# Kernel optimization log

Measured on AMD Instinct MI355X. Metric: run time of the kernel, lower is better.

Reference implementation:

```python
import jax, jax.numpy as jnp
import numpy as np

IN_F, OUT_F = 64, 32
N = IN_F * OUT_F + OUT_F  # 2080 sampled parameters (weights + bias)
B, S = 8, 2048
SCALE_INIT = 1.0 * float(np.sqrt(2.0 / (IN_F + OUT_F)))


def setup_inputs() -> dict:
    key = jax.random.key(0)
    k_x, k_eps, k_loc, k_cov = jax.random.split(key, 4)
    x = jax.random.normal(k_x, (B, S, IN_F), dtype=jnp.float32)
    eps = jax.random.normal(k_eps, (B, S, N), dtype=jnp.float32)
    loc = 0.01 * jax.random.normal(k_loc, (N,), dtype=jnp.float32)
    logvar = jnp.full((N,), float(np.log(SCALE_INIT)), dtype=jnp.float32)
    n_off = N * (N - 1) // 2
    cov_flat = 0.001 * jax.random.normal(k_cov, (n_off,), dtype=jnp.float32)
    return {"x": x, "eps": eps, "loc": loc, "logvar": logvar, "cov_flat": cov_flat}


def reference(x, eps, loc, logvar, cov_flat):
    n = loc.shape[0]
    in_f = x.shape[-1]
    out_f = n // (in_f + 1)  # n = out*(in+1)
    # flat_to_triangular (strictly lower) + make_cholesky, vectorized scatter
    rows, cols = np.tril_indices(n, -1)
    A = jnp.zeros((n, n), dtype=x.dtype).at[rows, cols].set(cov_flat)
    L = A + jnp.diag(jnp.exp(logvar * 0.5))  # off-diag from cov, diag = std
    # MultivariateNormal rsample: loc + L @ eps (per batch sample)
    W = loc + jnp.einsum('bsn,mn->bsm', eps, L)  # [B,S,N]
    b = W[..., :out_f]
    Wm = W[..., out_f:].reshape(*W.shape[:-1], in_f, out_f)  # [B,S,in,out]
    y = jnp.einsum('bsh,bshk->bsk', x, Wm) + b
    return y
```

## Files before the change

### kernel.cpp

```cpp
#include <hip/hip_runtime.h>
#include <hip/hip_bf16.h>

#define IN_F  64
#define OUT_F 32
#define NV    2080
#define NPAD  2176
#define MM    16384
#define KK    2080
#define NBN   17

typedef __attribute__((ext_vector_type(4))) float f32x4;
typedef __bf16 bf16x8 __attribute__((ext_vector_type(8)));

using gas_ptr = const __attribute__((address_space(1))) void*;
using lds_ptr = __attribute__((address_space(3))) void*;

__global__ __launch_bounds__(256) void build_L_k(const float* __restrict__ cov,
                                                 const float* __restrict__ logvar,
                                                 __hip_bfloat16* __restrict__ LB) {
    const int idx = blockIdx.x * 256 + threadIdx.x;
    const int m = idx / KK;
    const int k = idx - m * KK;
    float v = 0.0f;
    if (m < NV) {
        if (k < m)       v = cov[(size_t)(m * (m - 1) / 2) + k];
        else if (k == m) v = expf(0.5f * logvar[m]);
    }
    LB[idx] = __float2bfloat16(v);
}

__global__ __launch_bounds__(256) void gemm_zl_k(const float* __restrict__ A,
                                                 const __hip_bfloat16* __restrict__ BT,
                                                 const float* __restrict__ loc,
                                                 const float* __restrict__ x,
                                                 float* __restrict__ Ypart) {
    __shared__ __align__(16) __hip_bfloat16 As[2][128 * 32];
    __shared__ __align__(16) __hip_bfloat16 Bs[2][128 * 32];
    __shared__ float xs[128][4];

    const int tid  = threadIdx.x;
    const int bm   = blockIdx.x;
    const int bn   = (NBN - 1) - blockIdx.y;
    const int wave = tid >> 6;
    const int lane = tid & 63;
    const int quad = lane >> 4;
    const int r16  = lane & 15;

    const int kblocks = min(KK / 32, 4 * bn + 4);

    {
        const int tl = tid >> 1;
        const int cc = (tid & 1) * 2;
#pragma unroll
        for (int c = cc; c < cc + 2; c++) {
            const int h = 4 * bn - 1 + c;
            float w = 0.0f;
            if (bn == 0 && c == 0)          w = 1.0f;
            else if (h >= 0 && h < IN_F)    w = x[(size_t)(bm * 128 + tl) * IN_F + h];
            xs[tl][c] = w;
        }
    }

    const float*          Ag = A  + (size_t)bm * 128 * KK;
    const __hip_bfloat16* Bg = BT + (size_t)bn * 128 * KK;

    const int c0 = tid, c1 = tid + 256;
    const int ar0 = c0 >> 2, ap0 = (c0 & 3) ^ ((ar0 >> 1) & 3);
    const int ar1 = c1 >> 2, ap1 = (c1 & 3) ^ ((ar1 >> 1) & 3);
    const size_t gofs0 = (size_t)ar0 * KK + ap0 * 8;
    const size_t gofs1 = (size_t)ar1 * KK + ap1 * 8;

    f32x4 acc[2][8];
#pragma unroll
    for (int i = 0; i < 2; i++)
#pragma unroll
        for (int j = 0; j < 8; j++) acc[i][j] = f32x4{0.f, 0.f, 0.f, 0.f};

    int aofs[2], bofs[8];
#pragma unroll
    for (int i = 0; i < 2; i++) {
        const int arow = 32 * wave + 16 * i + r16;
        aofs[i] = arow * 32 + (quad ^ ((arow >> 1) & 3)) * 8;
    }
#pragma unroll
    for (int j = 0; j < 8; j++) {
        const int brow = 16 * j + r16;
        bofs[j] = brow * 32 + (quad ^ ((brow >> 1) & 3)) * 8;
    }

    {
        f32x4 ra0 = *(const f32x4*)(Ag + gofs0);
        f32x4 ra1 = *(const f32x4*)(Ag + gofs0 + 4);
        f32x4 ra2 = *(const f32x4*)(Ag + gofs1);
        f32x4 ra3 = *(const f32x4*)(Ag + gofs1 + 4);
        __builtin_amdgcn_global_load_lds((gas_ptr)(Bg + gofs0), (lds_ptr)(&Bs[0][0] + c0 * 8), 16, 0, 0);
        __builtin_amdgcn_global_load_lds((gas_ptr)(Bg + gofs1), (lds_ptr)(&Bs[0][0] + c1 * 8), 16, 0, 0);
        bf16x8 w0, w1;
#pragma unroll
        for (int q = 0; q < 4; q++) {
            w0[q] = (__bf16)ra0[q]; w0[4 + q] = (__bf16)ra1[q];
            w1[q] = (__bf16)ra2[q]; w1[4 + q] = (__bf16)ra3[q];
        }
        *(bf16x8*)(&As[0][0] + c0 * 8) = w0;
        *(bf16x8*)(&As[0][0] + c1 * 8) = w1;
    }

    for (int kb = 0; kb < kblocks; ++kb) {
        const int cur = kb & 1;
        __syncthreads();

        const bool pf = (kb + 1 < kblocks);
        f32x4 ra0, ra1, ra2, ra3;
        if (pf) {
            const size_t k0 = (size_t)(kb + 1) * 32;
            ra0 = *(const f32x4*)(Ag + k0 + gofs0);
            ra1 = *(const f32x4*)(Ag + k0 + gofs0 + 4);
            ra2 = *(const f32x4*)(Ag + k0 + gofs1);
            ra3 = *(const f32x4*)(Ag + k0 + gofs1 + 4);
            __builtin_amdgcn_global_load_lds((gas_ptr)(Bg + k0 + gofs0), (lds_ptr)(&Bs[cur ^ 1][0] + c0 * 8), 16, 0, 0);
            __builtin_amdgcn_global_load_lds((gas_ptr)(Bg + k0 + gofs1), (lds_ptr)(&Bs[cur ^ 1][0] + c1 * 8), 16, 0, 0);
        }

        bf16x8 af[2], bfr[8];
#pragma unroll
        for (int i = 0; i < 2; i++) af[i]  = *(const bf16x8*)(&As[cur][0] + aofs[i]);
#pragma unroll
        for (int j = 0; j < 8; j++) bfr[j] = *(const bf16x8*)(&Bs[cur][0] + bofs[j]);
#pragma unroll
        for (int i = 0; i < 2; i++)
#pragma unroll
            for (int j = 0; j < 8; j++)
                acc[i][j] = __builtin_amdgcn_mfma_f32_16x16x32_bf16(af[i], bfr[j], acc[i][j], 0, 0, 0);

        if (pf) {
            bf16x8 w0, w1;
#pragma unroll
            for (int q = 0; q < 4; q++) {
                w0[q] = (__bf16)ra0[q]; w0[4 + q] = (__bf16)ra1[q];
                w1[q] = (__bf16)ra2[q]; w1[4 + q] = (__bf16)ra3[q];
            }
            *(bf16x8*)(&As[cur ^ 1][0] + c0 * 8) = w0;
            *(bf16x8*)(&As[cur ^ 1][0] + c1 * 8) = w1;
        }
    }

    float locv[8];
#pragma unroll
    for (int j = 0; j < 8; j++) {
        const int col = bn * 128 + 16 * j + r16;
        locv[j] = (col < NV) ? loc[col] : 0.0f;
    }

    float* yp = Ypart + ((size_t)bn * MM + (size_t)bm * 128) * OUT_F;
#pragma unroll
    for (int i = 0; i < 2; i++) {
#pragma unroll
        for (int r = 0; r < 4; r++) {
            const int tl = 32 * wave + 16 * i + 4 * quad + r;
            float v0 = 0.0f, v1 = 0.0f;
#pragma unroll
            for (int c = 0; c < 4; c++) {
                const float w = xs[tl][c];
                v0 += w * (acc[i][2 * c][r]     + locv[2 * c]);
                v1 += w * (acc[i][2 * c + 1][r] + locv[2 * c + 1]);
            }
            yp[(size_t)tl * OUT_F + r16]      = v0;
            yp[(size_t)tl * OUT_F + 16 + r16] = v1;
        }
    }
}

__global__ __launch_bounds__(256) void reduce_y_k(const float4* __restrict__ yp,
                                                  float4* __restrict__ y) {
    const size_t i = (size_t)blockIdx.x * 256 + threadIdx.x;
    float4 s = yp[i];
#pragma unroll
    for (int b = 1; b < NBN; b++) {
        float4 v = yp[i + (size_t)b * (MM * OUT_F / 4)];
        s.x += v.x; s.y += v.y; s.z += v.z; s.w += v.w;
    }
    y[i] = s;
}

extern "C" void kernel_launch(void* const* d_in, const int* in_sizes, int n_in,
                              void* d_out, int out_size, void* d_ws, size_t ws_size,
                              hipStream_t stream) {
    const float* x      = (const float*)d_in[0];
    const float* eps    = (const float*)d_in[1];
    const float* loc    = (const float*)d_in[2];
    const float* logvar = (const float*)d_in[3];
    const float* cov    = (const float*)d_in[4];
    float* y = (float*)d_out;

    char* ws = (char*)d_ws;
    __hip_bfloat16* LB    = (__hip_bfloat16*)ws;
    float*          Ypart = (float*)(ws + (size_t)NPAD * KK * 2);

    build_L_k<<<(NPAD * KK) / 256, 256, 0, stream>>>(cov, logvar, LB);
    gemm_zl_k<<<dim3(MM / 128, NBN), 256, 0, stream>>>(eps, LB, loc, x, Ypart);
    reduce_y_k<<<(MM * OUT_F / 4) / 256, 256, 0, stream>>>((const float4*)Ypart, (float4*)y);
}
```

Measured before the change: 316.0 us.

## Deepen A-tile register prefetch, swap grid order, add occupancy hint

The fp32 A (eps) loads now run two k-blocks ahead through a pair of register sets, with the loop unrolled by two, so global latency has a full iteration more to hide. The bf16 conversion and LDS store for the next block now happen right after the barrier rather than after the MFMAs. The grid is transposed so that blocks sharing one eps row-tile (all bn for a given bm) launch next to each other, which should improve L2 reuse of the large eps stream. launch_bounds gains a minimum of 4 blocks per CU, which can limit registers and risk spills.

```diff
diff --git a/kernel.cpp b/kernel.cpp
--- a/kernel.cpp
+++ b/kernel.cpp
@@ -29,18 +29,18 @@
     LB[idx] = __float2bfloat16(v);
 }
 
-__global__ __launch_bounds__(256) void gemm_zl_k(const float* __restrict__ A,
-                                                 const __hip_bfloat16* __restrict__ BT,
-                                                 const float* __restrict__ loc,
-                                                 const float* __restrict__ x,
-                                                 float* __restrict__ Ypart) {
+__global__ __launch_bounds__(256, 4) void gemm_zl_k(const float* __restrict__ A,
+                                                    const __hip_bfloat16* __restrict__ BT,
+                                                    const float* __restrict__ loc,
+                                                    const float* __restrict__ x,
+                                                    float* __restrict__ Ypart) {
     __shared__ __align__(16) __hip_bfloat16 As[2][128 * 32];
     __shared__ __align__(16) __hip_bfloat16 Bs[2][128 * 32];
     __shared__ float xs[128][4];
 
     const int tid  = threadIdx.x;
-    const int bm   = blockIdx.x;
-    const int bn   = (NBN - 1) - blockIdx.y;
+    const int bn   = (NBN - 1) - blockIdx.x;
+    const int bm   = blockIdx.y;
     const int wave = tid >> 6;
     const int lane = tid & 63;
     const int quad = lane >> 4;
@@ -88,61 +88,76 @@
         bofs[j] = brow * 32 + (quad ^ ((brow >> 1) & 3)) * 8;
     }
 
+    f32x4 sa0, sa1, sa2, sa3;
+    f32x4 sb0, sb1, sb2, sb3;
+
     {
-        f32x4 ra0 = *(const f32x4*)(Ag + gofs0);
-        f32x4 ra1 = *(const f32x4*)(Ag + gofs0 + 4);
-        f32x4 ra2 = *(const f32x4*)(Ag + gofs1);
-        f32x4 ra3 = *(const f32x4*)(Ag + gofs1 + 4);
+        sa0 = *(const f32x4*)(Ag + gofs0);
+        sa1 = *(const f32x4*)(Ag + gofs0 + 4);
+        sa2 = *(const f32x4*)(Ag + gofs1);
+        sa3 = *(const f32x4*)(Ag + gofs1 + 4);
         __builtin_amdgcn_global_load_lds((gas_ptr)(Bg + gofs0), (lds_ptr)(&Bs[0][0] + c0 * 8), 16, 0, 0);
         __builtin_amdgcn_global_load_lds((gas_ptr)(Bg + gofs1), (lds_ptr)(&Bs[0][0] + c1 * 8), 16, 0, 0);
         bf16x8 w0, w1;
 #pragma unroll
         for (int q = 0; q < 4; q++) {
-            w0[q] = (__bf16)ra0[q]; w0[4 + q] = (__bf16)ra1[q];
-            w1[q] = (__bf16)ra2[q]; w1[4 + q] = (__bf16)ra3[q];
+            w0[q] = (__bf16)sa0[q]; w0[4 + q] = (__bf16)sa1[q];
+            w1[q] = (__bf16)sa2[q]; w1[4 + q] = (__bf16)sa3[q];
         }
         *(bf16x8*)(&As[0][0] + c0 * 8) = w0;
         *(bf16x8*)(&As[0][0] + c1 * 8) = w1;
-    }
-
-    for (int kb = 0; kb < kblocks; ++kb) {
-        const int cur = kb & 1;
-        __syncthreads();
-
-        const bool pf = (kb + 1 < kblocks);
-        f32x4 ra0, ra1, ra2, ra3;
-        if (pf) {
-            const size_t k0 = (size_t)(kb + 1) * 32;
-            ra0 = *(const f32x4*)(Ag + k0 + gofs0);
-            ra1 = *(const f32x4*)(Ag + k0 + gofs0 + 4);
-            ra2 = *(const f32x4*)(Ag + k0 + gofs1);
-            ra3 = *(const f32x4*)(Ag + k0 + gofs1 + 4);
-            __builtin_amdgcn_global_load_lds((gas_ptr)(Bg + k0 + gofs0), (lds_ptr)(&Bs[cur ^ 1][0] + c0 * 8), 16, 0, 0);
-            __builtin_amdgcn_global_load_lds((gas_ptr)(Bg + k0 + gofs1), (lds_ptr)(&Bs[cur ^ 1][0] + c1 * 8), 16, 0, 0);
-        }
-
-        bf16x8 af[2], bfr[8];
-#pragma unroll
-        for (int i = 0; i < 2; i++) af[i]  = *(const bf16x8*)(&As[cur][0] + aofs[i]);
-#pragma unroll
-        for (int j = 0; j < 8; j++) bfr[j] = *(const bf16x8*)(&Bs[cur][0] + bofs[j]);
-#pragma unroll
-        for (int i = 0; i < 2; i++)
-#pragma unroll
-            for (int j = 0; j < 8; j++)
-                acc[i][j] = __builtin_amdgcn_mfma_f32_16x16x32_bf16(af[i], bfr[j], acc[i][j], 0, 0, 0);
-
-        if (pf) {
-            bf16x8 w0, w1;
-#pragma unroll
-            for (int q = 0; q < 4; q++) {
-                w0[q] = (__bf16)ra0[q]; w0[4 + q] = (__bf16)ra1[q];
-                w1[q] = (__bf16)ra2[q]; w1[4 + q] = (__bf16)ra3[q];
-            }
-            *(bf16x8*)(&As[cur ^ 1][0] + c0 * 8) = w0;
-            *(bf16x8*)(&As[cur ^ 1][0] + c1 * 8) = w1;
-        }
-    }
+        if (1 < kblocks) {
+            sb0 = *(const f32x4*)(Ag + 32 + gofs0);
+            sb1 = *(const f32x4*)(Ag + 32 + gofs0 + 4);
+            sb2 = *(const f32x4*)(Ag + 32 + gofs1);
+            sb3 = *(const f32x4*)(Ag + 32 + gofs1 + 4);
+        }
+    }
+
+#define KSTEP(KB, CUR, W0, W1, W2, W3, L0, L1, L2, L3)                          \
+    {                                                                           \
+        __syncthreads();                                                        \
+        if ((KB) + 1 < kblocks) {                                               \
+            bf16x8 w0, w1;                                                      \
+            _Pragma("unroll")                                                   \
+            for (int q = 0; q < 4; q++) {                                       \
+                w0[q] = (__bf16)W0[q]; w0[4 + q] = (__bf16)W1[q];               \
+                w1[q] = (__bf16)W2[q]; w1[4 + q] = (__bf16)W3[q];               \
+            }                                                                   \
+            *(bf16x8*)(&As[(CUR) ^ 1][0] + c0 * 8) = w0;                        \
+            *(bf16x8*)(&As[(CUR) ^ 1][0] + c1 * 8) = w1;                        \
+            const size_t k1 = (size_t)((KB) + 1) * 32;                          \
+            __builtin_amdgcn_global_load_lds((gas_ptr)(Bg + k1 + gofs0),        \
+                (lds_ptr)(&Bs[(CUR) ^ 1][0] + c0 * 8), 16, 0, 0);               \
+            __builtin_amdgcn_global_load_lds((gas_ptr)(Bg + k1 + gofs1),        \
+                (lds_ptr)(&Bs[(CUR) ^ 1][0] + c1 * 8), 16, 0, 0);               \
+        }                                                                       \
+        if ((KB) + 2 < kblocks) {                                               \
+            const size_t k2 = (size_t)((KB) + 2) * 32;                          \
+            L0 = *(const f32x4*)(Ag + k2 + gofs0);                              \
+            L1 = *(const f32x4*)(Ag + k2 + gofs0 + 4);                          \
+            L2 = *(const f32x4*)(Ag + k2 + gofs1);                              \
+            L3 = *(const f32x4*)(Ag + k2 + gofs1 + 4);                          \
+        }                                                                       \
+        bf16x8 af[2], bfr[8];                                                   \
+        _Pragma("unroll")                                                       \
+        for (int i = 0; i < 2; i++) af[i]  = *(const bf16x8*)(&As[CUR][0] + aofs[i]); \
+        _Pragma("unroll")                                                       \
+        for (int j = 0; j < 8; j++) bfr[j] = *(const bf16x8*)(&Bs[CUR][0] + bofs[j]); \
+        _Pragma("unroll")                                                       \
+        for (int i = 0; i < 2; i++)                                             \
+            _Pragma("unroll")                                                   \
+            for (int j = 0; j < 8; j++)                                         \
+                acc[i][j] = __builtin_amdgcn_mfma_f32_16x16x32_bf16(af[i], bfr[j], acc[i][j], 0, 0, 0); \
+    }
+
+    for (int kb = 0; kb < kblocks; kb += 2) {
+        KSTEP(kb, 0, sb0, sb1, sb2, sb3, sa0, sa1, sa2, sa3);
+        if (kb + 1 < kblocks) {
+            KSTEP(kb + 1, 1, sa0, sa1, sa2, sa3, sb0, sb1, sb2, sb3);
+        }
+    }
+#undef KSTEP
 
     float locv[8];
 #pragma unroll
@@ -197,6 +212,6 @@
     float*          Ypart = (float*)(ws + (size_t)NPAD * KK * 2);
 
     build_L_k<<<(NPAD * KK) / 256, 256, 0, stream>>>(cov, logvar, LB);
-    gemm_zl_k<<<dim3(MM / 128, NBN), 256, 0, stream>>>(eps, LB, loc, x, Ypart);
+    gemm_zl_k<<<dim3(NBN, MM / 128), 256, 0, stream>>>(eps, LB, loc, x, Ypart);
     reduce_y_k<<<(MM * OUT_F / 4) / 256, 256, 0, stream>>>((const float4*)Ypart, (float4*)y);
 }
```

Measured after the change: 627.6 us. 98.6% more time.
